# Performance work log

Hardware: AMD Instinct MI355X
Metric: run time of the kernel (lower is better)

The kernel has to match this reference:

```python
import jax, jax.numpy as jnp
import numpy as np

K = 3  # de_neighbors
NUM_STAGES = 4


def _square_distance(a, b):
    # a: [B,N,3], b: [B,S,3] -> [B,N,S] squared euclidean distances
    return (jnp.sum(a * a, -1)[:, :, None]
            + jnp.sum(b * b, -1)[:, None, :]
            - 2.0 * jnp.einsum('bnd,bsd->bns', a, b))


def _propagate(xyz1, xyz2, points1, points2, k):
    # xyz1: [B,N,3] fine coords; xyz2: [B,S,3] coarse coords
    # points1: [B,C1,N] skip feats (or None); points2: [B,C2,S] coarse feats
    p2 = jnp.transpose(points2, (0, 2, 1))  # [B,S,C2]
    N = xyz1.shape[1]
    S = xyz2.shape[1]
    if S == 1:
        interp = jnp.tile(p2, (1, N, 1))
    else:
        d = _square_distance(xyz1, xyz2)            # [B,N,S]
        neg_d, idx = jax.lax.top_k(-d, k)           # k smallest dists
        dk = -neg_d                                 # [B,N,k]
        w = 1.0 / (dk + 1e-8)
        w = w / jnp.sum(w, axis=-1, keepdims=True)  # [B,N,k]
        gathered = jax.vmap(lambda p, i: p[i])(p2, idx)  # [B,N,k,C2]
        interp = jnp.sum(gathered * w[..., None], axis=2)  # [B,N,C2]
    if points1 is not None:
        interp = jnp.concatenate([jnp.transpose(points1, (0, 2, 1)), interp], axis=-1)
    return jnp.transpose(interp, (0, 2, 1))  # [B,C1+C2,N]


def setup_inputs() -> dict:
    key = jax.random.key(0)
    ks = jax.random.split(key, 10)
    B = 16
    Ns = [4096, 1024, 256, 64, 16]
    Cs = [64, 128, 256, 512, 1024]
    out = {}
    for i in range(5):
        out[f'xyz{i}'] = jax.random.normal(ks[i], (B, Ns[i], 3), dtype=jnp.float32)
        out[f'f{i}'] = jax.random.normal(ks[5 + i], (B, Cs[i], Ns[i]), dtype=jnp.float32)
    return out


def reference(xyz0, xyz1, xyz2, xyz3, xyz4, f0, f1, f2, f3, f4):
    # forward() reverses the fine->coarse lists to coarse->fine
    xyz = [xyz4, xyz3, xyz2, xyz1, xyz0]
    feats = [f4, f3, f2, f1, f0]
    x = feats[0]
    for i in range(NUM_STAGES):
        x = _propagate(xyz[i + 1], xyz[i], feats[i + 1], x, K)
    return x  # [B, 1984, 4096]
```

## Files before the change

### kernel.cpp

```cpp
#include <hip/hip_runtime.h>

#define B 16
typedef float f32x4 __attribute__((ext_vector_type(4)));

__device__ __forceinline__ void unpack_pw(const f32x4 pw, int& i0, int& i1, int& i2) {
    unsigned p = __float_as_uint(pw[0]);
    i0 = p & 1023; i1 = (p >> 10) & 1023; i2 = p >> 20;
}

__global__ __launch_bounds__(256) void knn_all_kernel(
    const float* __restrict__ xyz0, const float* __restrict__ xyz1,
    const float* __restrict__ xyz2, const float* __restrict__ xyz3,
    const float* __restrict__ xyz4, const float* __restrict__ f0,
    float* __restrict__ out,
    f32x4* pw0, f32x4* pw1, f32x4* pw2, f32x4* pw3) {
    __shared__ float lds[(256 + 1) * 4 * 4];
    int bid = blockIdx.x;
    if (bid >= 1360) {
        bid -= 1360;
        const int b = bid >> 3;
        const int c0 = (bid & 7) * 8;
        const f32x4* src = reinterpret_cast<const f32x4*>(f0 + ((size_t)b * 64 + c0) * 4096);
        f32x4* dst = reinterpret_cast<f32x4*>(out + ((size_t)b * 1984 + c0) * 4096);
        for (int i = threadIdx.x; i < 8 * 1024; i += 256) {
            __builtin_nontemporal_store(__builtin_nontemporal_load(src + i), dst + i);
        }
        return;
    }
    int S, logS4;
    const float *xf, *xc;
    f32x4* po;
    if (bid < 1024)      { S = 1024; logS4 = 8; xf = xyz0; xc = xyz1; po = pw3; }
    else if (bid < 1280) { bid -= 1024; S = 256; logS4 = 6; xf = xyz1; xc = xyz2; po = pw2; }
    else if (bid < 1344) { bid -= 1280; S = 64;  logS4 = 4; xf = xyz2; xc = xyz3; po = pw1; }
    else                 { bid -= 1344; S = 16;  logS4 = 2; xf = xyz3; xc = xyz4; po = pw0; }
    const int N = S << 2;
    const int lognb = logS4 - 2;
    const int b = bid >> lognb;
    const int nblk = bid & ((1 << lognb) - 1);
    const int S4 = S >> 2;

    const float* cbase = xc + (size_t)b * S * 3;
    for (int j = threadIdx.x; j < S; j += 256) {
        float x = cbase[j * 3 + 0], y = cbase[j * 3 + 1], z = cbase[j * 3 + 2];
        int seg = j >> logS4, jj = j & (S4 - 1);
        float* p = lds + (size_t)(seg * (S4 + 1) + jj) * 4;
        p[0] = x; p[1] = y; p[2] = z; p[3] = x * x + y * y + z * z;
    }
    __syncthreads();
    const int t = threadIdx.x;
    const int sub = t & 3;
    const int n = nblk * 64 + (t >> 2);
    const float* fp = xf + ((size_t)b * N + n) * 3;
    const float ax = fp[0], ay = fp[1], az = fp[2];
    const float an2 = ax * ax + ay * ay + az * az;
    float d0 = 1e30f, d1 = 1e30f, d2 = 1e30f;
    int i0 = -1, i1 = -1, i2 = -1;
    const f32x4* seg4 = reinterpret_cast<const f32x4*>(lds) + sub * (S4 + 1);
    const int jbase = sub * S4;
#pragma unroll 4
    for (int k = 0; k < S4; ++k) {
        f32x4 c = seg4[k];
        float d = an2 + c[3] - 2.0f * (ax * c[0] + ay * c[1] + az * c[2]);
        int j = jbase + k;
        if (d < d2) {
            if (d < d1) {
                d2 = d1; i2 = i1;
                if (d < d0) { d1 = d0; i1 = i0; d0 = d; i0 = j; }
                else        { d1 = d;  i1 = j; }
            } else { d2 = d; i2 = j; }
        }
    }
#pragma unroll
    for (int r = 1; r <= 2; r <<= 1) {
        float e0 = __shfl_xor(d0, r), e1 = __shfl_xor(d1, r), e2 = __shfl_xor(d2, r);
        int   j0 = __shfl_xor(i0, r), j1 = __shfl_xor(i1, r), j2 = __shfl_xor(i2, r);
        float ed[3] = {e0, e1, e2};
        int   ej[3] = {j0, j1, j2};
#pragma unroll
        for (int m = 0; m < 3; ++m) {
            float d = ed[m]; int j = ej[m];
            if (d < d0 || (d == d0 && j < i0)) {
                d2 = d1; i2 = i1; d1 = d0; i1 = i0; d0 = d; i0 = j;
            } else if (d < d1 || (d == d1 && j < i1)) {
                d2 = d1; i2 = i1; d1 = d; i1 = j;
            } else if (d < d2 || (d == d2 && j < i2)) {
                d2 = d; i2 = j;
            }
        }
    }
    if (sub == 0) {
        float w0_ = 1.0f / (d0 + 1e-8f);
        float w1_ = 1.0f / (d1 + 1e-8f);
        float w2_ = 1.0f / (d2 + 1e-8f);
        float inv = 1.0f / (w0_ + w1_ + w2_);
        unsigned packed = (unsigned)i0 | ((unsigned)i1 << 10) | ((unsigned)i2 << 20);
        f32x4 pw = {__uint_as_float(packed), w0_ * inv, w1_ * inv, w2_ * inv};
        po[(size_t)b * N + n] = pw;
    }
}


template <int P>
__device__ __forceinline__ void copy_plane(const float* __restrict__ src_rows,
                                           f32x4* dst, int t) {
    constexpr int P4 = P / 4;
    const f32x4* src = reinterpret_cast<const f32x4*>(src_rows);
    float* df = reinterpret_cast<float*>(dst);
    for (int e = t; e < 4 * P4; e += 256) {
        int c = e / P4;
        int s4 = e & (P4 - 1);
        f32x4 v = src[c * P4 + s4];
        int base = ((s4 * 4) << 2) + c;
        df[base + 0] = v[0]; df[base + 4] = v[1];
        df[base + 8] = v[2]; df[base + 12] = v[3];
    }
}

template <int PD, int PS>
__device__ __forceinline__ void expand(const f32x4* src, f32x4* dst,
                                       const f32x4* __restrict__ pwL,
                                       int b, int t) {
    for (int s = t; s < PD; s += 256) {
        f32x4 pw = pwL[(size_t)b * PD + s];
        int i0, i1, i2; unpack_pw(pw, i0, i1, i2);
        dst[s] = pw[1] * src[i0] + pw[2] * src[i1] + pw[3] * src[i2];
    }
}

__global__ __launch_bounds__(256, 8) void decode_kernel(
    const float* __restrict__ f1, const float* __restrict__ f2,
    const float* __restrict__ f3, const float* __restrict__ f4,
    const f32x4* __restrict__ pw0, const f32x4* __restrict__ pw1,
    const f32x4* __restrict__ pw2, const f32x4* __restrict__ pw3,
    float* __restrict__ out) {
    __shared__ f32x4 buf[1280];
    f32x4* s3 = buf;
    f32x4* s2 = buf + 1024;
    f32x4* s1 = buf;
    f32x4* s0 = buf + 64;
    const int b = blockIdx.x;
    const int cx = (479 - blockIdx.y) * 4;
    const int t = threadIdx.x;
    float* outb = out + ((size_t)b * 1984 + 64 + cx) * 4096;

    if (cx < 128) {
        copy_plane<1024>(f1 + ((size_t)b * 128 + cx) * 1024, s3, t);
        __syncthreads();
    } else if (cx < 384) {
        copy_plane<256>(f2 + ((size_t)b * 256 + (cx - 128)) * 256, s2, t);
        __syncthreads();
        expand<1024, 256>(s2, s3, pw2, b, t);
        __syncthreads();
    } else if (cx < 896) {
        copy_plane<64>(f3 + ((size_t)b * 512 + (cx - 384)) * 64, s1, t);
        __syncthreads();
        expand<256, 64>(s1, s2, pw1, b, t);
        __syncthreads();
        expand<1024, 256>(s2, s3, pw2, b, t);
        __syncthreads();
    } else {
        copy_plane<16>(f4 + ((size_t)b * 1024 + (cx - 896)) * 16, s0, t);
        __syncthreads();
        expand<64, 16>(s0, s1, pw0, b, t);
        __syncthreads();
        expand<256, 64>(s1, s2, pw1, b, t);
        __syncthreads();
        expand<1024, 256>(s2, s3, pw2, b, t);
        __syncthreads();
    }
    const f32x4* pwF = pw3 + (size_t)b * 4096;
#pragma unroll 2
    for (int it = 0; it < 4; ++it) {
        const int n0 = (it * 256 + t) * 4;
        f32x4 v[4];
#pragma unroll
        for (int q = 0; q < 4; ++q) {
            f32x4 pw = pwF[n0 + q];
            int i0, i1, i2; unpack_pw(pw, i0, i1, i2);
            v[q] = pw[1] * s3[i0] + pw[2] * s3[i1] + pw[3] * s3[i2];
        }
#pragma unroll
        for (int j = 0; j < 4; ++j) {
            f32x4 st = {v[0][j], v[1][j], v[2][j], v[3][j]};
            __builtin_nontemporal_store(st, reinterpret_cast<f32x4*>(outb + (size_t)j * 4096 + n0));
        }
    }
}

extern "C" void kernel_launch(void* const* d_in, const int* in_sizes, int n_in,
                              void* d_out, int out_size, void* d_ws, size_t ws_size,
                              hipStream_t stream) {
    static const int xyzSz[5] = {16 * 4096 * 3, 16 * 1024 * 3, 16 * 256 * 3,
                                 16 * 64 * 3, 16 * 16 * 3};
    static const int fSz[5] = {16 * 64 * 4096, 16 * 128 * 1024, 16 * 256 * 256,
                               16 * 512 * 64, 16 * 1024 * 16};
    const float* xyz[5] = {nullptr, nullptr, nullptr, nullptr, nullptr};
    const float* f[5] = {nullptr, nullptr, nullptr, nullptr, nullptr};
    for (int i = 0; i < n_in; ++i) {
        for (int j = 0; j < 5; ++j) {
            if (in_sizes[i] == xyzSz[j] && !xyz[j]) { xyz[j] = (const float*)d_in[i]; goto next; }
            if (in_sizes[i] == fSz[j] && !f[j])     { f[j] = (const float*)d_in[i];  goto next; }
        }
    next:;
    }

    char* ws = (char*)d_ws;
    f32x4* pw3 = (f32x4*)(ws);
    f32x4* pw2 = (f32x4*)(ws + (1u << 20));
    f32x4* pw1 = (f32x4*)(ws + (1u << 20) + 262144u);
    f32x4* pw0 = (f32x4*)(ws + (1u << 20) + 327680u);

    knn_all_kernel<<<1488, 256, 0, stream>>>(
        xyz[0], xyz[1], xyz[2], xyz[3], xyz[4], f[0], (float*)d_out,
        pw0, pw1, pw2, pw3);

    decode_kernel<<<dim3(B, 480), 256, 0, stream>>>(
        f[1], f[2], f[3], f[4], pw0, pw1, pw2, pw3, (float*)d_out);
}
```

Measured before the change: 135.2 us.

## Process eight channels per decode block to reuse neighbor weights across planes

Result: faster. 127.5 us (-5.7%).

```diff
diff --git a/kernel.cpp b/kernel.cpp
--- a/kernel.cpp
+++ b/kernel.cpp
@@ -102,16 +102,16 @@
 
 
 template <int P>
-__device__ __forceinline__ void copy_plane(const float* __restrict__ src_rows,
-                                           f32x4* dst, int t) {
+__device__ __forceinline__ void copy_planes(const float* __restrict__ src_rows,
+                                            f32x4* dst, int t) {
     constexpr int P4 = P / 4;
     const f32x4* src = reinterpret_cast<const f32x4*>(src_rows);
     float* df = reinterpret_cast<float*>(dst);
-    for (int e = t; e < 4 * P4; e += 256) {
+    for (int e = t; e < 8 * P4; e += 256) {
         int c = e / P4;
         int s4 = e & (P4 - 1);
         f32x4 v = src[c * P4 + s4];
-        int base = ((s4 * 4) << 2) + c;
+        int base = (((c >> 2) * P + s4 * 4) << 2) + (c & 3);
         df[base + 0] = v[0]; df[base + 4] = v[1];
         df[base + 8] = v[2]; df[base + 12] = v[3];
     }
@@ -121,46 +121,56 @@
 __device__ __forceinline__ void expand(const f32x4* src, f32x4* dst,
                                        const f32x4* __restrict__ pwL,
                                        int b, int t) {
-    for (int s = t; s < PD; s += 256) {
+    for (int e = t; e < 2 * PD; e += 256) {
+        int p = (e >= PD) ? 1 : 0;
+        int s = e - p * PD;
         f32x4 pw = pwL[(size_t)b * PD + s];
         int i0, i1, i2; unpack_pw(pw, i0, i1, i2);
-        dst[s] = pw[1] * src[i0] + pw[2] * src[i1] + pw[3] * src[i2];
-    }
-}
-
-__global__ __launch_bounds__(256, 8) void decode_kernel(
+        const f32x4* sp = src + p * PS;
+        dst[e] = pw[1] * sp[i0] + pw[2] * sp[i1] + pw[3] * sp[i2];
+    }
+}
+
+__global__ __launch_bounds__(256) void decode_kernel(
     const float* __restrict__ f1, const float* __restrict__ f2,
     const float* __restrict__ f3, const float* __restrict__ f4,
     const f32x4* __restrict__ pw0, const f32x4* __restrict__ pw1,
     const f32x4* __restrict__ pw2, const f32x4* __restrict__ pw3,
     float* __restrict__ out) {
-    __shared__ f32x4 buf[1280];
+    __shared__ f32x4 buf[2560];
     f32x4* s3 = buf;
-    f32x4* s2 = buf + 1024;
+    f32x4* s2 = buf + 2048;
     f32x4* s1 = buf;
-    f32x4* s0 = buf + 64;
+    f32x4* s0 = buf + 128;
     const int b = blockIdx.x;
-    const int cx = (479 - blockIdx.y) * 4;
+    const int y = blockIdx.y;
+    int c;
+    if (y < 16) c = 224 + y;
+    else {
+        int z = y - 16;
+        c = (z & 1) ? (z >> 1) : 112 + (z >> 1);
+    }
+    const int cx = c * 8;
     const int t = threadIdx.x;
     float* outb = out + ((size_t)b * 1984 + 64 + cx) * 4096;
 
     if (cx < 128) {
-        copy_plane<1024>(f1 + ((size_t)b * 128 + cx) * 1024, s3, t);
+        copy_planes<1024>(f1 + ((size_t)b * 128 + cx) * 1024, s3, t);
         __syncthreads();
     } else if (cx < 384) {
-        copy_plane<256>(f2 + ((size_t)b * 256 + (cx - 128)) * 256, s2, t);
+        copy_planes<256>(f2 + ((size_t)b * 256 + (cx - 128)) * 256, s2, t);
         __syncthreads();
         expand<1024, 256>(s2, s3, pw2, b, t);
         __syncthreads();
     } else if (cx < 896) {
-        copy_plane<64>(f3 + ((size_t)b * 512 + (cx - 384)) * 64, s1, t);
+        copy_planes<64>(f3 + ((size_t)b * 512 + (cx - 384)) * 64, s1, t);
         __syncthreads();
         expand<256, 64>(s1, s2, pw1, b, t);
         __syncthreads();
         expand<1024, 256>(s2, s3, pw2, b, t);
         __syncthreads();
     } else {
-        copy_plane<16>(f4 + ((size_t)b * 1024 + (cx - 896)) * 16, s0, t);
+        copy_planes<16>(f4 + ((size_t)b * 1024 + (cx - 896)) * 16, s0, t);
         __syncthreads();
         expand<64, 16>(s0, s1, pw0, b, t);
         __syncthreads();
@@ -173,17 +183,24 @@
 #pragma unroll 2
     for (int it = 0; it < 4; ++it) {
         const int n0 = (it * 256 + t) * 4;
-        f32x4 v[4];
-#pragma unroll
-        for (int q = 0; q < 4; ++q) {
-            f32x4 pw = pwF[n0 + q];
-            int i0, i1, i2; unpack_pw(pw, i0, i1, i2);
-            v[q] = pw[1] * s3[i0] + pw[2] * s3[i1] + pw[3] * s3[i2];
-        }
-#pragma unroll
-        for (int j = 0; j < 4; ++j) {
-            f32x4 st = {v[0][j], v[1][j], v[2][j], v[3][j]};
-            __builtin_nontemporal_store(st, reinterpret_cast<f32x4*>(outb + (size_t)j * 4096 + n0));
+        f32x4 pwv[4];
+#pragma unroll
+        for (int q = 0; q < 4; ++q) pwv[q] = pwF[n0 + q];
+#pragma unroll
+        for (int p = 0; p < 2; ++p) {
+            const f32x4* pl = s3 + p * 1024;
+            f32x4 v[4];
+#pragma unroll
+            for (int q = 0; q < 4; ++q) {
+                int i0, i1, i2; unpack_pw(pwv[q], i0, i1, i2);
+                v[q] = pwv[q][1] * pl[i0] + pwv[q][2] * pl[i1] + pwv[q][3] * pl[i2];
+            }
+            float* ob = outb + (size_t)(p * 4) * 4096 + n0;
+#pragma unroll
+            for (int j = 0; j < 4; ++j) {
+                f32x4 st = {v[0][j], v[1][j], v[2][j], v[3][j]};
+                __builtin_nontemporal_store(st, reinterpret_cast<f32x4*>(ob + (size_t)j * 4096));
+            }
         }
     }
 }
@@ -215,6 +232,6 @@
         xyz[0], xyz[1], xyz[2], xyz[3], xyz[4], f[0], (float*)d_out,
         pw0, pw1, pw2, pw3);
 
-    decode_kernel<<<dim3(B, 480), 256, 0, stream>>>(
+    decode_kernel<<<dim3(B, 240), 256, 0, stream>>>(
         f[1], f[2], f[3], f[4], pw0, pw1, pw2, pw3, (float*)d_out);
 }
```
